# Kernel optimization log

Measured on AMD Instinct MI355X. Metric: run time of the kernel, lower is better.

Reference implementation:

```python
import jax, jax.numpy as jnp
import numpy as np

EMBEDS = 512
HEADS = 4
HEAD_SIZE = 512  # head_size = embeds in Block.__init__
D_HEAD = EMBEDS // HEADS  # 128
LN_EPS = 512.0  # nn.LayerNorm(embeds, head_size) -> eps=head_size (faithful to source bug)
B, T = 4096, 4  # T must equal heads=4 for the mask broadcast in the source to work


def layer_norm(x, g, b, eps=LN_EPS):
    mu = jnp.mean(x, axis=-1, keepdims=True)
    var = jnp.mean(jnp.square(x - mu), axis=-1, keepdims=True)
    return (x - mu) / jnp.sqrt(var + eps) * g + b


def setup_inputs() -> dict:
    key = jax.random.key(0)
    ks = jax.random.split(key, 12)
    s_qkv = 1.0 / np.sqrt(D_HEAD)
    s_proj = 1.0 / np.sqrt(HEAD_SIZE)
    s_ff1 = 1.0 / np.sqrt(EMBEDS)
    s_ff2 = 1.0 / np.sqrt(4 * EMBEDS)
    return {
        "x": jax.random.normal(ks[0], (B, T, EMBEDS), dtype=jnp.float32),
        "Wq": jax.random.uniform(ks[1], (D_HEAD, HEAD_SIZE), jnp.float32, -s_qkv, s_qkv),
        "Wk": jax.random.uniform(ks[2], (D_HEAD, HEAD_SIZE), jnp.float32, -s_qkv, s_qkv),
        "Wv": jax.random.uniform(ks[3], (D_HEAD, HEAD_SIZE), jnp.float32, -s_qkv, s_qkv),
        "Wp": jax.random.uniform(ks[4], (HEAD_SIZE, EMBEDS), jnp.float32, -s_proj, s_proj),
        "bp": jax.random.uniform(ks[5], (EMBEDS,), jnp.float32, -s_proj, s_proj),
        "W1": jax.random.uniform(ks[6], (EMBEDS, 4 * EMBEDS), jnp.float32, -s_ff1, s_ff1),
        "b1": jax.random.uniform(ks[7], (4 * EMBEDS,), jnp.float32, -s_ff1, s_ff1),
        "W2": jax.random.uniform(ks[8], (4 * EMBEDS, EMBEDS), jnp.float32, -s_ff2, s_ff2),
        "b2": jax.random.uniform(ks[9], (EMBEDS,), jnp.float32, -s_ff2, s_ff2),
        "ln1_g": jnp.ones((EMBEDS,), jnp.float32),
        "ln1_b": jnp.zeros((EMBEDS,), jnp.float32),
        "ln2_g": jnp.ones((EMBEDS,), jnp.float32),
        "ln2_b": jnp.zeros((EMBEDS,), jnp.float32),
    }


def reference(x, Wq, Wk, Wv, Wp, bp, W1, b1, W2, b2, ln1_g, ln1_b, ln2_g, ln2_b):
    Bx, Tx, C = x.shape
    xh = x.reshape(Bx, Tx, HEADS, C // HEADS)          # [B,T,4,128]
    q = jnp.einsum('bthc,cd->bthd', xh, Wq)            # [B,T,4,512]
    k = jnp.einsum('bthc,cd->bthd', xh, Wk)
    v = jnp.einsum('bthc,cd->bthd', xh, Wv)
    # scores over the HEAD axis (faithful to source): [B,T,4,4]
    wei = jnp.einsum('btid,btjd->btij', q, k) * (HEAD_SIZE ** -0.5)
    causal = jnp.tril(jnp.ones((Tx, Tx), dtype=bool))  # broadcast over trailing [4,4]; requires T==4
    wei = jnp.where(causal, wei, -jnp.inf)
    wei = jax.nn.softmax(wei, axis=-1)                 # dropout omitted (eval mode)
    att = jnp.einsum('btij,btjd->btid', wei, v)        # [B,T,4,512]
    y = jnp.einsum('btid,de->btie', att, Wp) + bp      # [B,T,4,512]
    # residual broadcast: x [B,T,512] + y [B,T,4,512] -> [B,T,4,512]
    x1 = layer_norm(x[:, :, None, :] + y, ln1_g, ln1_b)
    h = jax.nn.gelu(jnp.einsum('btie,ef->btif', x1, W1) + b1, approximate=False)
    h = jnp.einsum('btif,fe->btie', h, W2) + b2
    return layer_norm(x1 + h, ln2_g, ln2_b)            # [B,T,4,512]
```

## Files before the change

kernel.cpp:

```cpp
#include <hip/hip_runtime.h>
#include <hip/hip_bf16.h>
#include <math.h>

typedef __bf16 bf16x8 __attribute__((ext_vector_type(8)));
typedef float f32x4 __attribute__((ext_vector_type(4)));
typedef unsigned short u16;
typedef unsigned int u32;
typedef u16 u16x4 __attribute__((ext_vector_type(4)));
typedef u16 u16x8 __attribute__((ext_vector_type(8)));

#define TOKENS 16384
#define MROWS  65536

__device__ __forceinline__ u16 f2bf(float f) {
  union { __hip_bfloat16 h; u16 u; } c;
  c.h = __float2bfloat16(f);
  return c.u;
}
__device__ __forceinline__ float bf2f(u16 u) {
  union { u16 u; __hip_bfloat16 h; } c;
  c.u = u;
  return __bfloat162float(c.h);
}
__device__ __forceinline__ float gelu_f(float u) {
  float y2 = u * fmaf(0.07135481283f, u * u, 1.595769122f);
  float e = __expf(-y2);
  return u / (1.f + e);
}
__device__ __forceinline__ void gload16(const void* g, void* l) {
  __builtin_amdgcn_global_load_lds(
      (const __attribute__((address_space(1))) void*)g,
      (__attribute__((address_space(3))) void*)l, 16, 0, 0);
}

__global__ void kprep_G(const float* __restrict__ Wq, const float* __restrict__ Wk,
                        u16* __restrict__ Gbf) {
  int id = blockIdx.x * 256 + threadIdx.x;
  int c = id >> 7, c2 = id & 127;
  const float4* a = (const float4*)(Wq + (size_t)c * 512);
  const float4* b = (const float4*)(Wk + (size_t)c2 * 512);
  float s = 0.f;
#pragma unroll 8
  for (int i = 0; i < 128; ++i) {
    float4 xa = a[i], yb = b[i];
    s += xa.x * yb.x + xa.y * yb.y + xa.z * yb.z + xa.w * yb.w;
  }
  Gbf[id] = f2bf(s * 0.044194173824159216f);
}

__global__ void kprep_Wvp(const float* __restrict__ Wv, const float* __restrict__ Wp,
                          u16* __restrict__ WvpT) {
  int id = blockIdx.x * 256 + threadIdx.x;
  int e = id >> 7, c = id & 127;
  float s = 0.f;
#pragma unroll 4
  for (int d = 0; d < 512; ++d) s += Wv[(size_t)c * 512 + d] * Wp[(size_t)d * 512 + e];
  WvpT[id] = f2bf(s);
}

__global__ __launch_bounds__(256) void kprep_W1T(const float* __restrict__ W1,
                                                 u16* __restrict__ W1T) {
  __shared__ u16 Lt[64][72];
  int tid = threadIdx.x;
  int bf = blockIdx.x, be = blockIdx.y;
#pragma unroll
  for (int rnd = 0; rnd < 4; ++rnd) {
    int r = rnd * 16 + (tid >> 4);
    int f4 = (tid & 15) * 4;
    float4 v = *(const float4*)(W1 + (size_t)(be * 64 + r) * 2048 + bf * 64 + f4);
    Lt[r][f4] = f2bf(v.x); Lt[r][f4 + 1] = f2bf(v.y);
    Lt[r][f4 + 2] = f2bf(v.z); Lt[r][f4 + 3] = f2bf(v.w);
  }
  __syncthreads();
  int fl = tid >> 2, eg = (tid & 3) * 16;
  u16x8 o0, o1;
#pragma unroll
  for (int q = 0; q < 8; ++q) { o0[q] = Lt[eg + q][fl]; o1[q] = Lt[eg + 8 + q][fl]; }
  u16* dst = W1T + (size_t)(bf * 64 + fl) * 512 + be * 64 + eg;
  *(u16x8*)dst = o0;
  *(u16x8*)(dst + 8) = o1;
}

__global__ __launch_bounds__(256) void kprep_W2T(const float* __restrict__ W2,
                                                 u16* __restrict__ W2T) {
  __shared__ u16 Lt[64][72];
  int tid = threadIdx.x;
  int bf = blockIdx.x, be = blockIdx.y;
#pragma unroll
  for (int rnd = 0; rnd < 4; ++rnd) {
    int r = rnd * 16 + (tid >> 4);
    int e4 = (tid & 15) * 4;
    float4 v = *(const float4*)(W2 + (size_t)(bf * 64 + r) * 512 + be * 64 + e4);
    Lt[r][e4] = f2bf(v.x); Lt[r][e4 + 1] = f2bf(v.y);
    Lt[r][e4 + 2] = f2bf(v.z); Lt[r][e4 + 3] = f2bf(v.w);
  }
  __syncthreads();
  int aa = bf & 1, fb = bf >> 1;
  int el = tid >> 2, g = tid & 3;
  u16x8 o0, o1;
#pragma unroll
  for (int q = 0; q < 8; ++q) {
    int fs0 = g * 16 + q, fs1 = g * 16 + 8 + q;
    o0[q] = Lt[(fs0 & 3) * 16 + ((fs0 >> 2) & 15)][el];
    o1[q] = Lt[(fs1 & 3) * 16 + ((fs1 >> 2) & 15)][el];
  }
  u16* dst = W2T + (size_t)(be * 64 + el) * 2048 + fb * 128 + aa * 64 + g * 16;
  *(u16x8*)dst = o0;
  *(u16x8*)(dst + 8) = o1;
}

__global__ __launch_bounds__(256) void ktoken(const float* __restrict__ x,
                                              const u16* __restrict__ Gbf,
                                              u16* __restrict__ Z) {
  __shared__ float Ss[4 * 512];
  __shared__ __align__(16) u16 Gs[16384];
  int tid = threadIdx.x;
  int wave = tid >> 6, lane = tid & 63;
  int tok = blockIdx.x * 4 + wave;
  char* GsC = (char*)Gs;
#pragma unroll
  for (int it = 0; it < 8; ++it)
    gload16(Gbf + (size_t)(it * 256 + tid) * 8, GsC + it * 4096 + wave * 1024);
  {
    const float4* xs = (const float4*)(x + (size_t)tok * 512);
    float4* sw = (float4*)(Ss + wave * 512);
    sw[lane] = xs[lane];
    sw[64 + lane] = xs[64 + lane];
  }
  __syncthreads();

  const float* Sw = Ss + wave * 512;
  const u32* Grow = (const u32*)Gs;
  float a[4][2] = {{0.f, 0.f}, {0.f, 0.f}, {0.f, 0.f}, {0.f, 0.f}};
#pragma unroll 4
  for (int c = 0; c < 128; ++c) {
    u32 g2 = Grow[c * 64 + lane];
    float glo = __uint_as_float(g2 << 16);
    float ghi = __uint_as_float(g2 & 0xFFFF0000u);
    float s0 = Sw[c], s1 = Sw[128 + c], s2 = Sw[256 + c], s3 = Sw[384 + c];
    a[0][0] += s0 * glo; a[0][1] += s0 * ghi;
    a[1][0] += s1 * glo; a[1][1] += s1 * ghi;
    a[2][0] += s2 * glo; a[2][1] += s2 * ghi;
    a[3][0] += s3 * glo; a[3][1] += s3 * ghi;
  }
  float w[16];
#pragma unroll
  for (int j = 0; j < 4; ++j) {
    float sj0 = Sw[j * 128 + 2 * lane];
    float sj1 = Sw[j * 128 + 2 * lane + 1];
#pragma unroll
    for (int i = 0; i < 4; ++i)
      w[i * 4 + j] = a[i][0] * sj0 + a[i][1] * sj1;
  }
#pragma unroll
  for (int off = 1; off < 64; off <<= 1)
#pragma unroll
    for (int k = 0; k < 16; ++k) w[k] += __shfl_xor(w[k], off);
  float p[4][4];
#pragma unroll
  for (int i = 0; i < 4; ++i) {
    float m = w[i * 4];
    for (int j = 1; j <= i; ++j) m = fmaxf(m, w[i * 4 + j]);
    float s = 0.f;
    for (int j = 0; j <= i; ++j) { p[i][j] = __expf(w[i * 4 + j] - m); s += p[i][j]; }
    float inv = 1.f / s;
    for (int j = 0; j <= i; ++j) p[i][j] *= inv;
    for (int j = i + 1; j < 4; ++j) p[i][j] = 0.f;
  }
  int c = lane * 2;
  u32* zout = (u32*)(Z + (size_t)tok * 512);
#pragma unroll
  for (int i = 0; i < 4; ++i) {
    float z0 = 0.f, z1 = 0.f;
#pragma unroll
    for (int j = 0; j < 4; ++j) {
      z0 += p[i][j] * Sw[j * 128 + c];
      z1 += p[i][j] * Sw[j * 128 + c + 1];
    }
    zout[i * 64 + lane] = (u32)f2bf(z0) | ((u32)f2bf(z1) << 16);
  }
}

__global__ __launch_bounds__(512) void kattn(const u16* __restrict__ Z,
                                             const u16* __restrict__ WvpT,
                                             const float* __restrict__ bp,
                                             const float* __restrict__ x,
                                             const float* __restrict__ g1,
                                             const float* __restrict__ bln1,
                                             u16* __restrict__ X1) {
  __shared__ __align__(16) u16 AO[32768];
  __shared__ float rsum[64 * 4];
  __shared__ float rsq[64 * 4];
  __shared__ float mus[64];
  __shared__ float rss[64];
  char* smem = (char*)AO;
  int tid = threadIdx.x;
  int lane = tid & 63, wid = tid >> 6;
  int wm = wid >> 2, wnq = wid & 3;
  int lane_lo = lane & 15, lane_hi = lane >> 4;
  int m0 = blockIdx.x * 64;
  {
    const u16* Zs = Z + (size_t)m0 * 128;
#pragma unroll
    for (int it = 0; it < 2; ++it) {
      int idx8 = it * 512 + tid;
      int row = idx8 >> 4, u = idx8 & 15;
      gload16(Zs + (size_t)row * 128 + ((u ^ (row & 7)) << 3), smem + idx8 * 16);
    }
    const float* xsrc = x + (size_t)(m0 >> 2) * 512;
#pragma unroll
    for (int it = 0; it < 4; ++it) {
      int idx = it * 512 + tid;
      gload16(xsrc + idx * 4, smem + 16384 + idx * 16);
    }
  }
  __syncthreads();
  f32x4 acc[2][8];
#pragma unroll
  for (int mi = 0; mi < 2; ++mi)
#pragma unroll
    for (int ni = 0; ni < 8; ++ni) acc[mi][ni] = (f32x4){0.f, 0.f, 0.f, 0.f};
#pragma unroll
  for (int ks = 0; ks < 4; ++ks) {
    bf16x8 af[2];
#pragma unroll
    for (int mi = 0; mi < 2; ++mi) {
      int row = wm * 32 + mi * 16 + lane_lo;
      int byte = (row * 256 + (ks * 32 + lane_hi * 8) * 2) ^ ((row & 7) << 4);
      af[mi] = *(const bf16x8*)(smem + byte);
    }
#pragma unroll
    for (int ni = 0; ni < 8; ++ni) {
      int n = wnq * 128 + ni * 16 + lane_lo;
      bf16x8 bfr = *(const bf16x8*)(WvpT + (size_t)n * 128 + ks * 32 + lane_hi * 8);
#pragma unroll
      for (int mi = 0; mi < 2; ++mi)
        acc[mi][ni] = __builtin_amdgcn_mfma_f32_16x16x32_bf16(af[mi], bfr, acc[mi][ni], 0, 0, 0);
    }
  }
  float bpv[8], g1v[8], blv[8];
#pragma unroll
  for (int ni = 0; ni < 8; ++ni) {
    int col = wnq * 128 + ni * 16 + lane_lo;
    bpv[ni] = bp[col]; g1v[ni] = g1[col]; blv[ni] = bln1[col];
  }
  const float* xs = (const float*)(smem + 16384);
#pragma unroll
  for (int mi = 0; mi < 2; ++mi) {
#pragma unroll
    for (int j = 0; j < 4; ++j) {
      int rl = wm * 32 + mi * 16 + lane_hi * 4 + j;
      int tl = wm * 8 + mi * 4 + lane_hi;
      float s = 0.f, q = 0.f;
#pragma unroll
      for (int ni = 0; ni < 8; ++ni) {
        int col = wnq * 128 + ni * 16 + lane_lo;
        float val = acc[mi][ni][j] + bpv[ni] + xs[tl * 512 + col];
        acc[mi][ni][j] = val;
        s += val; q += val * val;
      }
#pragma unroll
      for (int off = 1; off < 16; off <<= 1) { s += __shfl_xor(s, off); q += __shfl_xor(q, off); }
      if (lane_lo == 0) { rsum[rl * 4 + wnq] = s; rsq[rl * 4 + wnq] = q; }
    }
  }
  __syncthreads();
  if (tid < 64) {
    float s = rsum[tid * 4] + rsum[tid * 4 + 1] + rsum[tid * 4 + 2] + rsum[tid * 4 + 3];
    float q = rsq[tid * 4] + rsq[tid * 4 + 1] + rsq[tid * 4 + 2] + rsq[tid * 4 + 3];
    float mu = s * (1.f / 512.f);
    float var = q * (1.f / 512.f) - mu * mu;
    mus[tid] = mu;
    rss[tid] = rsqrtf(var + 512.0f);
  }
  __syncthreads();
#pragma unroll
  for (int mi = 0; mi < 2; ++mi) {
#pragma unroll
    for (int j = 0; j < 4; ++j) {
      int rl = wm * 32 + mi * 16 + lane_hi * 4 + j;
      float mu = mus[rl], rs = rss[rl];
#pragma unroll
      for (int ni = 0; ni < 8; ++ni) {
        int col = wnq * 128 + ni * 16 + lane_lo;
        AO[rl * 512 + col] = f2bf((acc[mi][ni][j] - mu) * rs * g1v[ni] + blv[ni]);
      }
    }
  }
  __syncthreads();
  {
    bf16x8* dst = (bf16x8*)(X1 + (size_t)m0 * 512);
    const bf16x8* s8 = (const bf16x8*)AO;
#pragma unroll
    for (int it = 0; it < 8; ++it) dst[it * 512 + tid] = s8[it * 512 + tid];
  }
}

template<int KDIM>
__device__ __forceinline__ void gemm_core_db(const u16* __restrict__ Ap,
                                             const u16* __restrict__ Bp,
                                             u16* AbBase, u16* BbBase,
                                             int wid, int lane, f32x4 acc[4][4]) {
  const int lane_lo = lane & 15, lane_hi = lane >> 4;
  const int wm = wid >> 1, wn = wid & 1;
  const int rl8 = lane >> 3, u8 = lane & 7;

  auto stage = [&](int buf, int k0) {
    char* AbC = (char*)AbBase + buf * 16384;
    char* BbC = (char*)BbBase + buf * 16384;
#pragma unroll
    for (int i = 0; i < 4; ++i) {
      int row = wid * 32 + i * 8 + rl8;
      int usw = u8 ^ (row & 7);
      size_t goff = (size_t)row * KDIM + k0 + usw * 8;
      gload16(Ap + goff, AbC + wid * 4096 + i * 1024);
      gload16(Bp + goff, BbC + wid * 4096 + i * 1024);
    }
  };
  auto compute = [&](int buf) {
    char* AbC = (char*)AbBase + buf * 16384;
    char* BbC = (char*)BbBase + buf * 16384;
#pragma unroll
    for (int ks = 0; ks < 2; ++ks) {
      bf16x8 av[4], bv[4];
#pragma unroll
      for (int mi = 0; mi < 4; ++mi) {
        int row = wm * 64 + mi * 16 + lane_lo;
        int usw = (ks * 4 + lane_hi) ^ (row & 7);
        av[mi] = *(const bf16x8*)(AbC + row * 128 + usw * 16);
      }
#pragma unroll
      for (int ni = 0; ni < 4; ++ni) {
        int row = wn * 64 + ni * 16 + lane_lo;
        int usw = (ks * 4 + lane_hi) ^ (row & 7);
        bv[ni] = *(const bf16x8*)(BbC + row * 128 + usw * 16);
      }
#pragma unroll
      for (int mi = 0; mi < 4; ++mi)
#pragma unroll
        for (int ni = 0; ni < 4; ++ni)
          acc[mi][ni] = __builtin_amdgcn_mfma_f32_16x16x32_bf16(av[mi], bv[ni], acc[mi][ni], 0, 0, 0);
    }
  };

  stage(0, 0);
  asm volatile("s_waitcnt vmcnt(0)" ::: "memory");
  __builtin_amdgcn_s_barrier();
  __builtin_amdgcn_sched_barrier(0);
  int cur = 0;
  for (int k0 = 64; k0 < KDIM; k0 += 64) {
    stage(cur ^ 1, k0);
    compute(cur);
    asm volatile("s_waitcnt vmcnt(0)" ::: "memory");
    __builtin_amdgcn_s_barrier();
    __builtin_amdgcn_sched_barrier(0);
    cur ^= 1;
  }
  compute(cur);
}

__global__ __launch_bounds__(512) void kff1(const u16* __restrict__ X1s,
                                            const u16* __restrict__ W1T,
                                            const float* __restrict__ b1v,
                                            u16* __restrict__ H) {
  __shared__ __align__(16) u16 Ab[16384];
  __shared__ __align__(16) u16 Bb[8192];
  char* AbC = (char*)Ab;
  char* BbC = (char*)Bb;
  int tid = threadIdx.x, lane = tid & 63, wid = tid >> 6;
  int lane_lo = lane & 15, lane_hi = lane >> 4;
  int wm = wid >> 1, wn = wid & 1;
  int rl8 = lane >> 3, u8 = lane & 7;
  int nwg = gridDim.x, bid = blockIdx.x;
  int m256 = nwg >> 4;
  int xcd = bid & 7, idx = bid >> 3;
  int mb = xcd * (m256 >> 3) + (idx >> 4);
  int nb = idx & 15;
  const u16* Ap = X1s + (size_t)mb * 256 * 512;
  const u16* Bp = W1T + (size_t)nb * 128 * 512;
  f32x4 acc[4][4];
#pragma unroll
  for (int mi = 0; mi < 4; ++mi)
#pragma unroll
    for (int ni = 0; ni < 4; ++ni) acc[mi][ni] = (f32x4){0.f, 0.f, 0.f, 0.f};

  for (int k0 = 0; k0 < 512; k0 += 64) {
#pragma unroll
    for (int i = 0; i < 4; ++i) {
      int row = wid * 32 + i * 8 + rl8;
      int usw = u8 ^ (row & 7);
      gload16(Ap + (size_t)row * 512 + k0 + usw * 8, AbC + wid * 4096 + i * 1024);
    }
#pragma unroll
    for (int i = 0; i < 2; ++i) {
      int row = wid * 16 + i * 8 + rl8;
      int usw = u8 ^ (row & 7);
      gload16(Bp + (size_t)row * 512 + k0 + usw * 8, BbC + wid * 2048 + i * 1024);
    }
    __syncthreads();
#pragma unroll
    for (int ks = 0; ks < 2; ++ks) {
      bf16x8 av[4], bv[4];
#pragma unroll
      for (int mi = 0; mi < 4; ++mi) {
        int row = wm * 64 + mi * 16 + lane_lo;
        int usw = (ks * 4 + lane_hi) ^ (row & 7);
        av[mi] = *(const bf16x8*)(AbC + row * 128 + usw * 16);
      }
#pragma unroll
      for (int ni = 0; ni < 4; ++ni) {
        int row = wn * 64 + ni * 16 + lane_lo;
        int usw = (ks * 4 + lane_hi) ^ (row & 7);
        bv[ni] = *(const bf16x8*)(BbC + row * 128 + usw * 16);
      }
#pragma unroll
      for (int mi = 0; mi < 4; ++mi)
#pragma unroll
        for (int ni = 0; ni < 4; ++ni)
          acc[mi][ni] = __builtin_amdgcn_mfma_f32_16x16x32_bf16(av[mi], bv[ni], acc[mi][ni], 0, 0, 0);
    }
    __syncthreads();
  }
  float bvals[4];
#pragma unroll
  for (int ni = 0; ni < 4; ++ni) bvals[ni] = b1v[nb * 128 + wn * 64 + ni * 16 + lane_lo];
  int colb = nb * 128 + (wn * 16 + lane_lo) * 4;
#pragma unroll
  for (int mi = 0; mi < 4; ++mi)
#pragma unroll
    for (int j = 0; j < 4; ++j) {
      int rl = wm * 64 + mi * 16 + lane_hi * 4 + j;
      u16x4 pk;
#pragma unroll
      for (int ni = 0; ni < 4; ++ni)
        pk[ni] = f2bf(gelu_f(acc[mi][ni][j] + bvals[ni]));
      *(u16x4*)(H + ((size_t)mb * 256 + rl) * 2048 + colb) = pk;
    }
}

__global__ __launch_bounds__(256) void kff2(const u16* __restrict__ H,
                                            const u16* __restrict__ W2T,
                                            const float* __restrict__ b2v,
                                            u16* __restrict__ X1y) {
  __shared__ __align__(16) u16 Ab[16384];
  __shared__ __align__(16) u16 Bb[16384];
  int tid = threadIdx.x, lane = tid & 63, wid = tid >> 6;
  int nwg = gridDim.x, bid = blockIdx.x;
  int m128 = nwg >> 2;
  int xcd = bid & 7, idx = bid >> 3;
  int mb = xcd * (m128 >> 3) + (idx >> 2);
  int nb = idx & 3;
  const u16* Ap = H + (size_t)mb * 128 * 2048;
  const u16* Bp = W2T + (size_t)nb * 128 * 2048;
  f32x4 acc[4][4];
#pragma unroll
  for (int mi = 0; mi < 4; ++mi)
#pragma unroll
    for (int ni = 0; ni < 4; ++ni) acc[mi][ni] = (f32x4){0.f, 0.f, 0.f, 0.f};
  gemm_core_db<2048>(Ap, Bp, Ab, Bb, wid, lane, acc);
  int lane_lo = lane & 15, lane_hi = lane >> 4;
  int wm = wid >> 1, wn = wid & 1;
#pragma unroll
  for (int mi = 0; mi < 4; ++mi)
#pragma unroll
    for (int j = 0; j < 4; ++j) {
      int rl = wm * 64 + mi * 16 + lane_hi * 4 + j;
      size_t row = (size_t)mb * 128 + rl;
      u16* xrow = X1y + row * 512 + nb * 128;
#pragma unroll
      for (int ni = 0; ni < 4; ++ni) {
        int col = wn * 64 + ni * 16 + lane_lo;
        float val = acc[mi][ni][j] + b2v[nb * 128 + col] + bf2f(xrow[col]);
        xrow[col] = f2bf(val);
      }
    }
}

__global__ __launch_bounds__(512) void kln2(const u16* __restrict__ Y,
                                            const float* __restrict__ g2,
                                            const float* __restrict__ bb2,
                                            float* __restrict__ out) {
  int wid = threadIdx.x >> 6, lane = threadIdx.x & 63;
  size_t row = (size_t)blockIdx.x * 8 + wid;
  u16x8 v = *(const u16x8*)(Y + row * 512 + lane * 8);
  float f[8];
  float s = 0.f, q = 0.f;
#pragma unroll
  for (int k = 0; k < 8; ++k) {
    f[k] = bf2f(v[k]);
    s += f[k]; q += f[k] * f[k];
  }
#pragma unroll
  for (int off = 1; off < 64; off <<= 1) { s += __shfl_xor(s, off); q += __shfl_xor(q, off); }
  float mu = s * (1.f / 512.f);
  float rs = rsqrtf(q * (1.f / 512.f) - mu * mu + 512.0f);
  float4 ga = *(const float4*)(g2 + lane * 8);
  float4 gb = *(const float4*)(g2 + lane * 8 + 4);
  float4 ba = *(const float4*)(bb2 + lane * 8);
  float4 bb = *(const float4*)(bb2 + lane * 8 + 4);
  float4 o0, o1;
  o0.x = (f[0] - mu) * rs * ga.x + ba.x;
  o0.y = (f[1] - mu) * rs * ga.y + ba.y;
  o0.z = (f[2] - mu) * rs * ga.z + ba.z;
  o0.w = (f[3] - mu) * rs * ga.w + ba.w;
  o1.x = (f[4] - mu) * rs * gb.x + bb.x;
  o1.y = (f[5] - mu) * rs * gb.y + bb.y;
  o1.z = (f[6] - mu) * rs * gb.z + bb.z;
  o1.w = (f[7] - mu) * rs * gb.w + bb.w;
  float* orow = out + row * 512 + lane * 8;
  *(float4*)orow = o0;
  *(float4*)(orow + 4) = o1;
}

extern "C" void kernel_launch(void* const* d_in, const int* in_sizes, int n_in,
                              void* d_out, int out_size, void* d_ws, size_t ws_size,
                              hipStream_t stream) {
  const float* x   = (const float*)d_in[0];
  const float* Wq  = (const float*)d_in[1];
  const float* Wk  = (const float*)d_in[2];
  const float* Wv  = (const float*)d_in[3];
  const float* Wp  = (const float*)d_in[4];
  const float* bp  = (const float*)d_in[5];
  const float* W1  = (const float*)d_in[6];
  const float* b1  = (const float*)d_in[7];
  const float* W2  = (const float*)d_in[8];
  const float* b2  = (const float*)d_in[9];
  const float* g1  = (const float*)d_in[10];
  const float* bb1 = (const float*)d_in[11];
  const float* g2  = (const float*)d_in[12];
  const float* bb2 = (const float*)d_in[13];
  float* out = (float*)d_out;

  char* ws = (char*)d_ws;
  u16* Gbf  = (u16*)ws;
  u16* WvpT = (u16*)(ws + (256 << 10));
  u16* W1T  = (u16*)(ws + (1 << 20));
  u16* W2T  = (u16*)(ws + (3 << 20));
  u16* Z    = (u16*)(ws + (5 << 20));
  u16* X1   = (u16*)(ws + (21 << 20));
  u16* H    = (u16*)(ws + (85ull << 20));

  hipLaunchKernelGGL(kprep_G,   dim3(64),        dim3(256), 0, stream, Wq, Wk, Gbf);
  hipLaunchKernelGGL(kprep_Wvp, dim3(256),       dim3(256), 0, stream, Wv, Wp, WvpT);
  hipLaunchKernelGGL(kprep_W1T, dim3(32, 8),     dim3(256), 0, stream, W1, W1T);
  hipLaunchKernelGGL(kprep_W2T, dim3(32, 8),     dim3(256), 0, stream, W2, W2T);
  hipLaunchKernelGGL(ktoken,    dim3(4096),      dim3(256), 0, stream, x, Gbf, Z);
  hipLaunchKernelGGL(kattn,     dim3(1024),      dim3(512), 0, stream, Z, WvpT, bp, x, g1, bb1, X1);

  const size_t hbase = 85ull << 20;
  int S = 64;
  for (int c = 4; c <= 64; c <<= 1) {
    if (hbase + (268435456ull / (size_t)c) <= ws_size) { S = c; break; }
  }
  int Ms = MROWS / S;
  for (int s = 0; s < S; ++s) {
    const u16* x1s = X1 + (size_t)s * Ms * 512;
    hipLaunchKernelGGL(kff1, dim3((Ms / 256) * 16), dim3(512), 0, stream, x1s, W1T, b1, H);
    hipLaunchKernelGGL(kff2, dim3((Ms / 128) * 4),  dim3(256), 0, stream, H, W2T, b2,
                       X1 + (size_t)s * Ms * 512);
  }
  hipLaunchKernelGGL(kln2, dim3(8192), dim3(512), 0, stream, X1, g2, bb2, out);
}
```

Measured before the change: 576.1 us.

## Use 256x128 tiles with 512 threads for FF2 and share the GEMM core with FF1

The FF2 GEMM moves from 128x128 tiles on 256 threads with a double-buffered LDS pipeline to 256x128 tiles on 512 threads with a single buffer and __syncthreads, the same shape FF1 already uses. Both kernels now call one shared gemm256 routine. Larger M tiles halve the number of times each W2T slice is re-read and reduce the block count. The trade is losing the overlap of global loads with MFMA compute that the double-buffered version had, and fewer blocks.

Result: slower. 599.1 us (+4.0%).

```diff
diff --git a/kernel.cpp b/kernel.cpp
--- a/kernel.cpp
+++ b/kernel.cpp
@@ -297,29 +297,29 @@
 }
 
 template<int KDIM>
-__device__ __forceinline__ void gemm_core_db(const u16* __restrict__ Ap,
-                                             const u16* __restrict__ Bp,
-                                             u16* AbBase, u16* BbBase,
-                                             int wid, int lane, f32x4 acc[4][4]) {
+__device__ __forceinline__ void gemm256(const u16* __restrict__ Ap,
+                                        const u16* __restrict__ Bp,
+                                        u16* Ab, u16* Bb,
+                                        int wid, int lane, f32x4 acc[4][4]) {
+  char* AbC = (char*)Ab;
+  char* BbC = (char*)Bb;
   const int lane_lo = lane & 15, lane_hi = lane >> 4;
   const int wm = wid >> 1, wn = wid & 1;
   const int rl8 = lane >> 3, u8 = lane & 7;
-
-  auto stage = [&](int buf, int k0) {
-    char* AbC = (char*)AbBase + buf * 16384;
-    char* BbC = (char*)BbBase + buf * 16384;
+  for (int k0 = 0; k0 < KDIM; k0 += 64) {
 #pragma unroll
     for (int i = 0; i < 4; ++i) {
       int row = wid * 32 + i * 8 + rl8;
       int usw = u8 ^ (row & 7);
-      size_t goff = (size_t)row * KDIM + k0 + usw * 8;
-      gload16(Ap + goff, AbC + wid * 4096 + i * 1024);
-      gload16(Bp + goff, BbC + wid * 4096 + i * 1024);
-    }
-  };
-  auto compute = [&](int buf) {
-    char* AbC = (char*)AbBase + buf * 16384;
-    char* BbC = (char*)BbBase + buf * 16384;
+      gload16(Ap + (size_t)row * KDIM + k0 + usw * 8, AbC + wid * 4096 + i * 1024);
+    }
+#pragma unroll
+    for (int i = 0; i < 2; ++i) {
+      int row = wid * 16 + i * 8 + rl8;
+      int usw = u8 ^ (row & 7);
+      gload16(Bp + (size_t)row * KDIM + k0 + usw * 8, BbC + wid * 2048 + i * 1024);
+    }
+    __syncthreads();
 #pragma unroll
     for (int ks = 0; ks < 2; ++ks) {
       bf16x8 av[4], bv[4];
@@ -341,22 +341,8 @@
         for (int ni = 0; ni < 4; ++ni)
           acc[mi][ni] = __builtin_amdgcn_mfma_f32_16x16x32_bf16(av[mi], bv[ni], acc[mi][ni], 0, 0, 0);
     }
-  };
-
-  stage(0, 0);
-  asm volatile("s_waitcnt vmcnt(0)" ::: "memory");
-  __builtin_amdgcn_s_barrier();
-  __builtin_amdgcn_sched_barrier(0);
-  int cur = 0;
-  for (int k0 = 64; k0 < KDIM; k0 += 64) {
-    stage(cur ^ 1, k0);
-    compute(cur);
-    asm volatile("s_waitcnt vmcnt(0)" ::: "memory");
-    __builtin_amdgcn_s_barrier();
-    __builtin_amdgcn_sched_barrier(0);
-    cur ^= 1;
-  }
-  compute(cur);
+    __syncthreads();
+  }
 }
 
 __global__ __launch_bounds__(512) void kff1(const u16* __restrict__ X1s,
@@ -365,12 +351,9 @@
                                             u16* __restrict__ H) {
   __shared__ __align__(16) u16 Ab[16384];
   __shared__ __align__(16) u16 Bb[8192];
-  char* AbC = (char*)Ab;
-  char* BbC = (char*)Bb;
   int tid = threadIdx.x, lane = tid & 63, wid = tid >> 6;
   int lane_lo = lane & 15, lane_hi = lane >> 4;
   int wm = wid >> 1, wn = wid & 1;
-  int rl8 = lane >> 3, u8 = lane & 7;
   int nwg = gridDim.x, bid = blockIdx.x;
   int m256 = nwg >> 4;
   int xcd = bid & 7, idx = bid >> 3;
@@ -383,44 +366,7 @@
   for (int mi = 0; mi < 4; ++mi)
 #pragma unroll
     for (int ni = 0; ni < 4; ++ni) acc[mi][ni] = (f32x4){0.f, 0.f, 0.f, 0.f};
-
-  for (int k0 = 0; k0 < 512; k0 += 64) {
-#pragma unroll
-    for (int i = 0; i < 4; ++i) {
-      int row = wid * 32 + i * 8 + rl8;
-      int usw = u8 ^ (row & 7);
-      gload16(Ap + (size_t)row * 512 + k0 + usw * 8, AbC + wid * 4096 + i * 1024);
-    }
-#pragma unroll
-    for (int i = 0; i < 2; ++i) {
-      int row = wid * 16 + i * 8 + rl8;
-      int usw = u8 ^ (row & 7);
-      gload16(Bp + (size_t)row * 512 + k0 + usw * 8, BbC + wid * 2048 + i * 1024);
-    }
-    __syncthreads();
-#pragma unroll
-    for (int ks = 0; ks < 2; ++ks) {
-      bf16x8 av[4], bv[4];
-#pragma unroll
-      for (int mi = 0; mi < 4; ++mi) {
-        int row = wm * 64 + mi * 16 + lane_lo;
-        int usw = (ks * 4 + lane_hi) ^ (row & 7);
-        av[mi] = *(const bf16x8*)(AbC + row * 128 + usw * 16);
-      }
-#pragma unroll
-      for (int ni = 0; ni < 4; ++ni) {
-        int row = wn * 64 + ni * 16 + lane_lo;
-        int usw = (ks * 4 + lane_hi) ^ (row & 7);
-        bv[ni] = *(const bf16x8*)(BbC + row * 128 + usw * 16);
-      }
-#pragma unroll
-      for (int mi = 0; mi < 4; ++mi)
-#pragma unroll
-        for (int ni = 0; ni < 4; ++ni)
-          acc[mi][ni] = __builtin_amdgcn_mfma_f32_16x16x32_bf16(av[mi], bv[ni], acc[mi][ni], 0, 0, 0);
-    }
-    __syncthreads();
-  }
+  gemm256<512>(Ap, Bp, Ab, Bb, wid, lane, acc);
   float bvals[4];
 #pragma unroll
   for (int ni = 0; ni < 4; ++ni) bvals[ni] = b1v[nb * 128 + wn * 64 + ni * 16 + lane_lo];
@@ -438,34 +384,34 @@
     }
 }
 
-__global__ __launch_bounds__(256) void kff2(const u16* __restrict__ H,
+__global__ __launch_bounds__(512) void kff2(const u16* __restrict__ H,
                                             const u16* __restrict__ W2T,
                                             const float* __restrict__ b2v,
                                             u16* __restrict__ X1y) {
   __shared__ __align__(16) u16 Ab[16384];
-  __shared__ __align__(16) u16 Bb[16384];
+  __shared__ __align__(16) u16 Bb[8192];
   int tid = threadIdx.x, lane = tid & 63, wid = tid >> 6;
+  int lane_lo = lane & 15, lane_hi = lane >> 4;
+  int wm = wid >> 1, wn = wid & 1;
   int nwg = gridDim.x, bid = blockIdx.x;
-  int m128 = nwg >> 2;
+  int m256 = nwg >> 2;
   int xcd = bid & 7, idx = bid >> 3;
-  int mb = xcd * (m128 >> 3) + (idx >> 2);
+  int mb = xcd * (m256 >> 3) + (idx >> 2);
   int nb = idx & 3;
-  const u16* Ap = H + (size_t)mb * 128 * 2048;
+  const u16* Ap = H + (size_t)mb * 256 * 2048;
   const u16* Bp = W2T + (size_t)nb * 128 * 2048;
   f32x4 acc[4][4];
 #pragma unroll
   for (int mi = 0; mi < 4; ++mi)
 #pragma unroll
     for (int ni = 0; ni < 4; ++ni) acc[mi][ni] = (f32x4){0.f, 0.f, 0.f, 0.f};
-  gemm_core_db<2048>(Ap, Bp, Ab, Bb, wid, lane, acc);
-  int lane_lo = lane & 15, lane_hi = lane >> 4;
-  int wm = wid >> 1, wn = wid & 1;
+  gemm256<2048>(Ap, Bp, Ab, Bb, wid, lane, acc);
 #pragma unroll
   for (int mi = 0; mi < 4; ++mi)
 #pragma unroll
     for (int j = 0; j < 4; ++j) {
       int rl = wm * 64 + mi * 16 + lane_hi * 4 + j;
-      size_t row = (size_t)mb * 128 + rl;
+      size_t row = (size_t)mb * 256 + rl;
       u16* xrow = X1y + row * 512 + nb * 128;
 #pragma unroll
       for (int ni = 0; ni < 4; ++ni) {
@@ -556,7 +502,7 @@
   for (int s = 0; s < S; ++s) {
     const u16* x1s = X1 + (size_t)s * Ms * 512;
     hipLaunchKernelGGL(kff1, dim3((Ms / 256) * 16), dim3(512), 0, stream, x1s, W1T, b1, H);
-    hipLaunchKernelGGL(kff2, dim3((Ms / 128) * 4),  dim3(256), 0, stream, H, W2T, b2,
+    hipLaunchKernelGGL(kff2, dim3((Ms / 256) * 4),  dim3(512), 0, stream, H, W2T, b2,
                        X1 + (size_t)s * Ms * 512);
   }
   hipLaunchKernelGGL(kln2, dim3(8192), dim3(512), 0, stream, X1, g2, bb2, out);
```
